# Optimization experiments

Hardware: AMD Instinct MI355X
Metric: run time of the kernel (lower is better)

Reference implementation:

```python
import jax, jax.numpy as jnp
import numpy as np

E = 16   # experts (== in_channel, forced by the gate/one_hot structure)
K = 2    # top_k

def _conv(x, w, b, pad):
    y = jax.lax.conv_general_dilated(x, w, (1, 1), pad,
                                     dimension_numbers=('NCHW', 'OIHW', 'NCHW'))
    return y + b[None, :, None, None]

def setup_inputs() -> dict:
    key = jax.random.key(0)
    ks = jax.random.split(key, 5)
    B, Cin, H, W = 8, 16, 128, 128
    Cout = 64
    return {
        'x': jax.random.normal(ks[0], (B, Cin, H, W), jnp.float32),
        'gate_w': jax.random.normal(ks[1], (Cin, Cin, 1, 1), jnp.float32) * 0.1,
        'gate_b': jax.random.normal(ks[2], (Cin,), jnp.float32) * 0.1,
        'expert_w': jax.random.normal(ks[3], (E, Cout, Cin, 3, 3), jnp.float32) * 0.05,
        'expert_b': jax.random.normal(ks[4], (E, Cout), jnp.float32) * 0.05,
    }

def reference(x, gate_w, gate_b, expert_w, expert_b):
    B, Cin, H, W = x.shape
    # ---- router ----
    logits = _conv(x, gate_w, gate_b, 'VALID')            # [B, E, H, W] (1x1 conv)
    probs = jax.nn.softmax(logits.astype(jnp.float32), axis=1)
    p_last = jnp.moveaxis(probs, 1, -1)                   # [B, H, W, E]
    w, idx = jax.lax.top_k(p_last, K)                     # [B, H, W, K]
    w = w / jnp.sum(w, axis=-1, keepdims=True)
    w = jnp.moveaxis(w, -1, 1).astype(x.dtype)            # [B, K, H, W]
    idx = jnp.moveaxis(idx, -1, 1)                        # [B, K, H, W]
    # ---- run all experts densely (one big conv), then routed weighted sum ----
    Ew = expert_w.reshape(E * expert_w.shape[1], Cin, 3, 3)
    Eb = expert_b.reshape(-1)
    all_out = _conv(x, Ew, Eb, 'SAME')                    # [B, E*Cout, H, W]
    Cout = expert_w.shape[1]
    all_out = all_out.reshape(B, E, Cout, H, W)
    # gather routed experts (equivalent to sum over one-hot mask * expert output)
    gidx = idx[:, :, None, :, :]                          # [B, K, 1, H, W]
    sel = jnp.take_along_axis(all_out, jnp.broadcast_to(gidx, (B, K, Cout, H, W)), axis=1)
    out = jnp.sum(sel * w[:, :, None, :, :], axis=1)      # [B, Cout, H, W]
    return out, logits
```

## Files before the change

### kernel.cpp

```cpp
#include <hip/hip_runtime.h>
#include <cmath>

typedef __attribute__((ext_vector_type(8))) short bf16x8;
typedef __attribute__((ext_vector_type(4))) float f32x4;

static __device__ __forceinline__ unsigned int f2bf(float f) {
    union { float f; unsigned int u; } v; v.f = f;
    unsigned int r = v.u + 0x7FFFu + ((v.u >> 16) & 1u);
    return r >> 16;
}

__global__ __launch_bounds__(256) void prep_w_kernel(const float* __restrict__ ew,
                                                     const float* __restrict__ eb,
                                                     unsigned short* __restrict__ wb) {
    const int c = blockIdx.x * 256 + threadIdx.x;
    if (c >= 20480) return;
    const int e    = c / 1280;
    const int r    = c - e * 1280;
    const int ks   = r >> 8;
    const int nf   = (r >> 6) & 3;
    const int quad = (r >> 4) & 3;
    const int lq   = r & 15;
    const int n    = nf * 16 + lq;
    const int k0   = ks * 32 + quad * 8;
    uint4 dv = make_uint4(0u, 0u, 0u, 0u);
    if (k0 <= 136) {
        const float* s = ew + (e * 64 + n) * 144 + k0;
        const float4 a  = *(const float4*)(s);
        const float4 cc = *(const float4*)(s + 4);
        dv.x = f2bf(a.x)  | (f2bf(a.y)  << 16);
        dv.y = f2bf(a.z)  | (f2bf(a.w)  << 16);
        dv.z = f2bf(cc.x) | (f2bf(cc.y) << 16);
        dv.w = f2bf(cc.z) | (f2bf(cc.w) << 16);
    } else if (k0 == 144) {
        dv.x = f2bf(eb[e * 64 + n]);
    }
    *(uint4*)(wb + c * 8) = dv;
}

__global__ __launch_bounds__(256, 2) void moe_dense_kernel(
    const float* __restrict__ x,
    const float* __restrict__ gw,
    const float* __restrict__ gb,
    const unsigned short* __restrict__ wb,
    float* __restrict__ out,
    float* __restrict__ logits_out)
{
    __shared__ __align__(16) unsigned short Ab[64 * 168];
    __shared__ __align__(16) float wexp[16 * 64];
    __shared__ float lg[64 * 17];
    __shared__ float outt[64 * 65];

    const int tid = threadIdx.x;
    const int b   = blockIdx.x >> 8;
    const int row = (blockIdx.x >> 1) & 127;
    const int px0 = (blockIdx.x & 1) << 6;

    const int lane = tid & 63;
    const int wave = tid >> 6;
    const int quad = lane >> 4;
    const int lq   = lane & 15;
    const int n    = lq + 16 * wave;

    for (int i = tid; i < 1024; i += 256) wexp[i] = 0.f;

    {
        const int px  = tid & 63;
        const int og  = tid >> 6;
        const int col = px0 + px;
        const float* xp = x + (b * 16) * 16384 + row * 128 + col;
        float xv[16];
        #pragma unroll
        for (int ci = 0; ci < 16; ++ci) xv[ci] = xp[ci * 16384];
        const int rbase = ((b * 16) * 128 + row) * 128 + col;
        #pragma unroll
        for (int j = 0; j < 4; ++j) {
            const int o = og * 4 + j;
            float acc = gb[o];
            #pragma unroll
            for (int i = 0; i < 16; ++i) acc += gw[o * 16 + i] * xv[i];
            lg[px * 17 + o] = acc;
            logits_out[rbase + o * 16384] = acc;
        }
    }

    {
        const int px  = tid & 63;
        const int s0  = tid >> 6;
        const int col = px0 + px;
        float xa[36];
        #pragma unroll
        for (int j = 0; j < 12; ++j) {
            const int s  = s0 + 4 * j;
            const int ci = s / 3;
            const int ky = s - ci * 3;
            int gr = row - 1 + ky;
            gr = gr < 0 ? 0 : (gr > 127 ? 127 : gr);
            const float* xr = x + ((b * 16 + ci) * 128 + gr) * 128;
            xa[3 * j + 0] = (col > 0)   ? xr[col - 1] : 0.f;
            xa[3 * j + 1] = xr[col];
            xa[3 * j + 2] = (col < 127) ? xr[col + 1] : 0.f;
        }
        #pragma unroll
        for (int j = 0; j < 12; ++j) {
            const int s  = s0 + 4 * j;
            const int ci = s / 3;
            const int ky = s - ci * 3;
            const int gr = row - 1 + ky;
            const bool ok = (gr >= 0) && (gr < 128);
            unsigned short* dst = Ab + px * 168 + ci * 9 + ky * 3;
            dst[0] = ok ? (unsigned short)f2bf(xa[3 * j + 0]) : (unsigned short)0;
            dst[1] = ok ? (unsigned short)f2bf(xa[3 * j + 1]) : (unsigned short)0;
            dst[2] = ok ? (unsigned short)f2bf(xa[3 * j + 2]) : (unsigned short)0;
        }
    }
    if (tid < 192) {
        const int px = tid / 3, h = tid - px * 3;
        uint4 pv = make_uint4(h == 0 ? 0x00003F80u : 0u, 0u, 0u, 0u);
        *(uint4*)(Ab + px * 168 + 144 + h * 8) = pv;
    }
    __syncthreads();

    if (tid < 64) {
        float l[16];
        #pragma unroll
        for (int o = 0; o < 16; ++o) l[o] = lg[tid * 17 + o];
        float m = l[0];
        #pragma unroll
        for (int o = 1; o < 16; ++o) m = fmaxf(m, l[o]);
        float p0 = expf(l[0] - m), p1 = -1.f;
        int i0 = 0, i1 = 0;
        #pragma unroll
        for (int o = 1; o < 16; ++o) {
            float pv = expf(l[o] - m);
            if (pv > p0)      { p1 = p0; i1 = i0; p0 = pv; i0 = o; }
            else if (pv > p1) { p1 = pv; i1 = o; }
        }
        const float ws = p0 + p1;
        wexp[i0 * 64 + tid] = p0 / ws;
        wexp[i1 * 64 + tid] = p1 / ws;
    }
    bf16x8 af[4][5];
    #pragma unroll
    for (int mt = 0; mt < 4; ++mt) {
        const unsigned short* arow = Ab + (mt * 16 + lq) * 168 + quad * 8;
        #pragma unroll
        for (int ks = 0; ks < 5; ++ks) af[mt][ks] = *(const bf16x8*)(arow + ks * 32);
    }
    #pragma unroll
    for (int mt = 0; mt < 4; ++mt)
        #pragma unroll
        for (int ks = 0; ks < 5; ++ks)
            asm volatile("" : "+v"(af[mt][ks]));
    __syncthreads();

    const unsigned short* bp = wb + wave * 512 + lane * 8;
    bf16x8 bn[5];
    #pragma unroll
    for (int ks = 0; ks < 5; ++ks) bn[ks] = *(const bf16x8*)(bp + ks * 2048);

    f32x4 facc[4] = {{0.f,0.f,0.f,0.f},{0.f,0.f,0.f,0.f},{0.f,0.f,0.f,0.f},{0.f,0.f,0.f,0.f}};

    for (int e = 0; e < 16; ++e) {
        bf16x8 bc[5];
        #pragma unroll
        for (int ks = 0; ks < 5; ++ks) bc[ks] = bn[ks];
        if (e < 15) {
            const unsigned short* p = bp + (e + 1) * 10240;
            #pragma unroll
            for (int ks = 0; ks < 5; ++ks) bn[ks] = *(const bf16x8*)(p + ks * 2048);
        }
        #pragma unroll
        for (int mt = 0; mt < 4; ++mt) {
            const f32x4 wv = *(const f32x4*)&wexp[e * 64 + mt * 16 + quad * 4];
            f32x4 acc = {0.f, 0.f, 0.f, 0.f};
            #pragma unroll
            for (int ks = 0; ks < 5; ++ks)
                acc = __builtin_amdgcn_mfma_f32_16x16x32_bf16(af[mt][ks], bc[ks], acc, 0, 0, 0);
            #pragma unroll
            for (int r = 0; r < 4; ++r)
                facc[mt][r] += wv[r] * acc[r];
        }
    }

    #pragma unroll
    for (int mt = 0; mt < 4; ++mt)
        #pragma unroll
        for (int r = 0; r < 4; ++r)
            outt[(mt * 16 + quad * 4 + r) * 65 + n] = facc[mt][r];
    __syncthreads();
    for (int i = tid; i < 4096; i += 256) {
        const int c = i >> 6, px = i & 63;
        out[((b * 64 + c) * 128 + row) * 128 + px0 + px] = outt[px * 65 + c];
    }
}

extern "C" void kernel_launch(void* const* d_in, const int* in_sizes, int n_in,
                              void* d_out, int out_size, void* d_ws, size_t ws_size,
                              hipStream_t stream) {
    const float* x  = (const float*)d_in[0];
    const float* gw = (const float*)d_in[1];
    const float* gb = (const float*)d_in[2];
    const float* ew = (const float*)d_in[3];
    const float* eb = (const float*)d_in[4];
    float* out        = (float*)d_out;
    float* logits_out = out + 8 * 64 * 128 * 128;
    unsigned short* wb = (unsigned short*)d_ws;

    prep_w_kernel<<<dim3(80), dim3(256), 0, stream>>>(ew, eb, wb);
    moe_dense_kernel<<<dim3(2048), dim3(256), 0, stream>>>(
        x, gw, gb, wb, out, logits_out);
}
```

Baseline: 121.1 us.

## Fuse weight prep and MoE compute into one cooperative persistent kernel

Replaces the two-kernel launch (weight conversion then dense MoE) with a single cooperative kernel of 512 blocks. Each block converts a slice of the expert weights to bf16, then a grid-wide sync runs before every block processes four tiles in a persistent loop. The aim is to remove one kernel launch and the gap between the two kernels. In exchange it adds a grid barrier, reduces the grid from 2048 to 512 blocks so tail and latency hiding may change, and falls back to the old path if the cooperative launch fails.

New measurement: 294.8 us. 143% more time.

```diff
diff --git a/kernel.cpp b/kernel.cpp
--- a/kernel.cpp
+++ b/kernel.cpp
@@ -1,5 +1,8 @@
 #include <hip/hip_runtime.h>
+#include <hip/hip_cooperative_groups.h>
 #include <cmath>
+
+namespace cg = cooperative_groups;
 
 typedef __attribute__((ext_vector_type(8))) short bf16x8;
 typedef __attribute__((ext_vector_type(4))) float f32x4;
@@ -10,11 +13,9 @@
     return r >> 16;
 }
 
-__global__ __launch_bounds__(256) void prep_w_kernel(const float* __restrict__ ew,
-                                                     const float* __restrict__ eb,
-                                                     unsigned short* __restrict__ wb) {
-    const int c = blockIdx.x * 256 + threadIdx.x;
-    if (c >= 20480) return;
+static __device__ __forceinline__ void prep_chunk(int c, const float* __restrict__ ew,
+                                                  const float* __restrict__ eb,
+                                                  unsigned short* __restrict__ wb) {
     const int e    = c / 1280;
     const int r    = c - e * 1280;
     const int ks   = r >> 8;
@@ -38,7 +39,12 @@
     *(uint4*)(wb + c * 8) = dv;
 }
 
-__global__ __launch_bounds__(256, 2) void moe_dense_kernel(
+static __device__ __forceinline__ void process_tile(
+    int tileIdx,
+    unsigned short* __restrict__ Ab,
+    float* __restrict__ wexp,
+    float* __restrict__ lg,
+    float* __restrict__ outt,
     const float* __restrict__ x,
     const float* __restrict__ gw,
     const float* __restrict__ gb,
@@ -46,15 +52,10 @@
     float* __restrict__ out,
     float* __restrict__ logits_out)
 {
-    __shared__ __align__(16) unsigned short Ab[64 * 168];
-    __shared__ __align__(16) float wexp[16 * 64];
-    __shared__ float lg[64 * 17];
-    __shared__ float outt[64 * 65];
-
     const int tid = threadIdx.x;
-    const int b   = blockIdx.x >> 8;
-    const int row = (blockIdx.x >> 1) & 127;
-    const int px0 = (blockIdx.x & 1) << 6;
+    const int b   = tileIdx >> 8;
+    const int row = (tileIdx >> 1) & 127;
+    const int px0 = (tileIdx & 1) << 6;
 
     const int lane = tid & 63;
     const int wave = tid >> 6;
@@ -193,6 +194,46 @@
         const int c = i >> 6, px = i & 63;
         out[((b * 64 + c) * 128 + row) * 128 + px0 + px] = outt[px * 65 + c];
     }
+}
+
+__global__ __launch_bounds__(256, 2) void moe_coop_kernel(
+    const float* __restrict__ x, const float* __restrict__ gw,
+    const float* __restrict__ gb, const float* __restrict__ ew,
+    const float* __restrict__ eb, unsigned short* __restrict__ wb,
+    float* __restrict__ out, float* __restrict__ logits_out)
+{
+    __shared__ __align__(16) unsigned short Ab[64 * 168];
+    __shared__ __align__(16) float wexp[16 * 64];
+    __shared__ float lg[64 * 17];
+    __shared__ float outt[64 * 65];
+
+    if (threadIdx.x < 40)
+        prep_chunk(blockIdx.x * 40 + threadIdx.x, ew, eb, wb);
+    cg::this_grid().sync();
+
+    #pragma unroll 1
+    for (int t = 0; t < 4; ++t)
+        process_tile(t * 512 + blockIdx.x, Ab, wexp, lg, outt,
+                     x, gw, gb, wb, out, logits_out);
+}
+
+__global__ __launch_bounds__(256) void prep_w_kernel(const float* __restrict__ ew,
+                                                     const float* __restrict__ eb,
+                                                     unsigned short* __restrict__ wb) {
+    const int c = blockIdx.x * 256 + threadIdx.x;
+    if (c < 20480) prep_chunk(c, ew, eb, wb);
+}
+
+__global__ __launch_bounds__(256, 2) void moe_dense_kernel(
+    const float* __restrict__ x, const float* __restrict__ gw,
+    const float* __restrict__ gb, const unsigned short* __restrict__ wb,
+    float* __restrict__ out, float* __restrict__ logits_out)
+{
+    __shared__ __align__(16) unsigned short Ab[64 * 168];
+    __shared__ __align__(16) float wexp[16 * 64];
+    __shared__ float lg[64 * 17];
+    __shared__ float outt[64 * 65];
+    process_tile(blockIdx.x, Ab, wexp, lg, outt, x, gw, gb, wb, out, logits_out);
 }
 
 extern "C" void kernel_launch(void* const* d_in, const int* in_sizes, int n_in,
@@ -207,7 +248,14 @@
     float* logits_out = out + 8 * 64 * 128 * 128;
     unsigned short* wb = (unsigned short*)d_ws;
 
-    prep_w_kernel<<<dim3(80), dim3(256), 0, stream>>>(ew, eb, wb);
-    moe_dense_kernel<<<dim3(2048), dim3(256), 0, stream>>>(
-        x, gw, gb, wb, out, logits_out);
-}
+    void* args[] = { (void*)&x, (void*)&gw, (void*)&gb, (void*)&ew,
+                     (void*)&eb, (void*)&wb, (void*)&out, (void*)&logits_out };
+    hipError_t err = hipLaunchCooperativeKernel((const void*)moe_coop_kernel,
+                                                dim3(512), dim3(256), args, 0, stream);
+    if (err != hipSuccess) {
+        (void)hipGetLastError();
+        prep_w_kernel<<<dim3(80), dim3(256), 0, stream>>>(ew, eb, wb);
+        moe_dense_kernel<<<dim3(2048), dim3(256), 0, stream>>>(
+            x, gw, gb, wb, out, logits_out);
+    }
+}
```
